# Kernel tuning notes

Hardware: AMD Instinct MI355X
Metric: run time of the kernel (lower is better)

Reference implementation:

```python
import jax, jax.numpy as jnp
import numpy as np

T = 0.07  # temperature from __init__ default


def setup_inputs() -> dict:
    key = jax.random.key(0)
    ks = jax.random.split(key, 5)
    B, D, H, E = 4096, 2048, 2048, 128
    init = lambda k, shp, fan: jax.random.normal(k, shp, dtype=jnp.float32) * (1.0 / np.sqrt(fan))
    return {
        "input1": jax.random.normal(ks[0], (B, D), dtype=jnp.float32),
        "input2": jax.random.normal(ks[1], (B, D), dtype=jnp.float32),
        "W0": init(ks[2], (D, H), D), "b0": jnp.zeros((H,), jnp.float32),
        "W1": init(ks[3], (H, H), H), "b1": jnp.zeros((H,), jnp.float32),
        "W2": init(ks[4], (H, E), H), "b2": jnp.zeros((E,), jnp.float32),
    }


def _mlp(x, W0, b0, W1, b1, W2, b2):
    # Linear -> ReLU -> Linear -> Linear (ReLU only between hidden layers)
    x = jax.nn.relu(x @ W0 + b0)
    x = x @ W1 + b1
    return x @ W2 + b2


def reference(input1, input2, W0, b0, W1, b1, W2, b2):
    B = input1.shape[0]
    e1 = _mlp(input1, W0, b0, W1, b1, W2, b2)
    e2 = _mlp(input2, W0, b0, W1, b1, W2, b2)
    feats = jnp.stack([e1, e2], axis=1)                       # [B, 2, E]
    feats = feats / jnp.linalg.norm(feats, axis=2, keepdims=True)
    # view(N,2,dim).permute(1,0,2).reshape(2N,dim): view0 rows then view1 rows
    f = jnp.concatenate([feats[:, 0], feats[:, 1]], axis=0)   # [2B, E]
    N2 = 2 * B
    sim = (f @ f.T) / T                                        # [2B, 2B]
    idx = jnp.arange(N2)
    pos = sim[idx, (idx + B) % N2]                             # partner view similarity
    # exclude self-similarity (diagonal) from the logsumexp denominator
    sim = jnp.where(jnp.eye(N2, dtype=bool), jnp.float32(-1e9), sim)
    # CE with positive at index 0 of [pos, negatives] == -pos + logsumexp(non-self)
    loss = jnp.mean(jax.nn.logsumexp(sim, axis=1) - pos)
    return loss
```

## Files before the change

kernel.cpp:

```cpp
#include <hip/hip_runtime.h>
#include <stdint.h>

typedef float f32x4 __attribute__((ext_vector_type(4)));
typedef float f32x16 __attribute__((ext_vector_type(16)));
typedef __bf16 bf16x8 __attribute__((ext_vector_type(8)));
typedef unsigned short u16;
typedef unsigned int u32;

#define INVT 14.285714285714286f

__device__ __forceinline__ u16 f2bf(float f) {
  u32 u = __float_as_uint(f);
  u32 r = (u + 0x7fffu + ((u >> 16) & 1u)) >> 16;
  return (u16)r;
}
__device__ __forceinline__ float bf2f(u16 h) { return __uint_as_float(((u32)h) << 16); }

__device__ __forceinline__ void g2l16(const void* g, void* l) {
  auto gp = reinterpret_cast<__attribute__((address_space(1))) uint32_t*>(
      reinterpret_cast<uintptr_t>(g));
  auto lp = reinterpret_cast<__attribute__((address_space(3))) uint32_t*>(
      reinterpret_cast<uintptr_t>(l));
  __builtin_amdgcn_global_load_lds(gp, lp, 16, 0, 0);
}

__global__ __launch_bounds__(256) void k_cvt2(const float* __restrict__ in1,
                                              const float* __restrict__ in2,
                                              u16* __restrict__ out) {
  int i = (blockIdx.x * 256 + threadIdx.x) * 4;
  float4 v;
  if (i < 8388608) v = *(const float4*)(in1 + i);
  else             v = *(const float4*)(in2 + (i - 8388608));
  ushort4 p;
  p.x = f2bf(v.x); p.y = f2bf(v.y); p.z = f2bf(v.z); p.w = f2bf(v.w);
  *(ushort4*)(out + i) = p;
}

__global__ __launch_bounds__(256) void k_transpose2(const float* __restrict__ w0,
                                                    u16* __restrict__ w0t,
                                                    const float* __restrict__ w1,
                                                    u16* __restrict__ w1t) {
  const float* in = blockIdx.z ? w1 : w0;
  u16* out = blockIdx.z ? w1t : w0t;
  const int R = 2048, C = 2048;
  __shared__ float t[64][65];
  const int r0 = blockIdx.y * 64, c0 = blockIdx.x * 64;
#pragma unroll
  for (int p = 0; p < 16; ++p) {
    int idx = p * 256 + threadIdx.x;
    int r = idx >> 6, c = idx & 63;
    t[r][c] = in[(size_t)(r0 + r) * C + (c0 + c)];
  }
  __syncthreads();
#pragma unroll
  for (int p = 0; p < 16; ++p) {
    int idx = p * 256 + threadIdx.x;
    int c = idx >> 6, r = idx & 63;
    out[(size_t)(c0 + c) * R + (r0 + r)] = f2bf(t[r][c]);
  }
}

__global__ __launch_bounds__(256) void k_transpose(const float* __restrict__ in,
                                                   u16* __restrict__ out, int R, int C) {
  __shared__ float t[64][65];
  const int r0 = blockIdx.y * 64, c0 = blockIdx.x * 64;
#pragma unroll
  for (int p = 0; p < 16; ++p) {
    int idx = p * 256 + threadIdx.x;
    int r = idx >> 6, c = idx & 63;
    t[r][c] = in[(size_t)(r0 + r) * C + (c0 + c)];
  }
  __syncthreads();
#pragma unroll
  for (int p = 0; p < 16; ++p) {
    int idx = p * 256 + threadIdx.x;
    int c = idx >> 6, r = idx & 63;
    out[(size_t)(c0 + c) * R + (r0 + r)] = f2bf(t[r][c]);
  }
}

__global__ __launch_bounds__(256, 2) void k_gemm(const u16* __restrict__ A, const u16* __restrict__ Bt,
                                                 const float* __restrict__ bias, u16* __restrict__ C,
                                                 int M, int N, int K, int relu) {
  __shared__ __align__(16) u16 sm[36864];
  const int tid = threadIdx.x;
  const int l = tid & 63, w = tid >> 6;
  const int wm = w >> 1, wn = w & 1;
  const int m0 = blockIdx.y * 256, n0 = blockIdx.x * 128;

  const int kb = ((l & 3) ^ ((l >> 3) & 3)) * 16;
  const char* gA = (const char*)(A + (size_t)(m0 + w * 64 + (l >> 2)) * K) + kb;
  const char* gB = (const char*)(Bt + (size_t)(n0 + w * 32 + (l >> 2)) * K) + kb;
  const size_t chRows = (size_t)16 * K * 2;

  auto issue = [&](int kcB, int stg) {
    char* base = (char*)sm + stg * 24576;
    char* dA = base + (w * 4) * 1024 + l * 16;
    char* dB = base + 16384 + (w * 2) * 1024 + l * 16;
#pragma unroll
    for (int j = 0; j < 4; ++j) g2l16(gA + j * chRows + kcB, dA + j * 1024);
#pragma unroll
    for (int j = 0; j < 2; ++j) g2l16(gB + j * chRows + kcB, dB + j * 1024);
  };

  const int lm = l & 31;
  const int c0 = l >> 5;
  const int sw = (lm >> 1) & 3;

  f32x16 acc[4][2] = {};

  auto compute = [&](int stg) {
    const u16* As = sm + stg * 12288;
    const u16* Bs = As + 8192;
#pragma unroll
    for (int t = 0; t < 2; ++t) {
      const int cc = (((t << 1) + c0) ^ sw) * 8;
      bf16x8 a4[4], b2[2];
#pragma unroll
      for (int fm = 0; fm < 4; ++fm)
        a4[fm] = *(const bf16x8*)(As + (wm * 128 + fm * 32 + lm) * 32 + cc);
#pragma unroll
      for (int fn = 0; fn < 2; ++fn)
        b2[fn] = *(const bf16x8*)(Bs + (wn * 64 + fn * 32 + lm) * 32 + cc);
#pragma unroll
      for (int fm = 0; fm < 4; ++fm)
#pragma unroll
        for (int fn = 0; fn < 2; ++fn)
          acc[fm][fn] = __builtin_amdgcn_mfma_f32_32x32x16_bf16(a4[fm], b2[fn],
                                                                acc[fm][fn], 0, 0, 0);
    }
  };

  const int NK = K >> 5;
  issue(0, 0);
  issue(64, 1);
  int st = 0;
  for (int kt = 0; kt < NK; ++kt) {
    if (kt + 1 < NK) asm volatile("s_waitcnt vmcnt(6)" ::: "memory");
    else             asm volatile("s_waitcnt vmcnt(0)" ::: "memory");
    asm volatile("s_barrier" ::: "memory");
    if (kt + 2 < NK) {
      int stp = st + 2; if (stp >= 3) stp -= 3;
      issue((kt + 2) * 64, stp);
    }
    compute(st);
    ++st; if (st == 3) st = 0;
  }

  const int colb = n0 + wn * 64 + lm;
  const int rowb = m0 + wm * 128 + 4 * c0;
#pragma unroll
  for (int fn = 0; fn < 2; ++fn) {
    const float b = bias[colb + fn * 32];
#pragma unroll
    for (int fm = 0; fm < 4; ++fm)
#pragma unroll
      for (int g = 0; g < 4; ++g)
#pragma unroll
        for (int rr = 0; rr < 4; ++rr) {
          float v = acc[fm][fn][g * 4 + rr] + b;
          if (relu) v = fmaxf(v, 0.0f);
          C[(size_t)(rowb + fm * 32 + g * 8 + rr) * N + colb + fn * 32] = f2bf(v);
        }
  }
}

__global__ __launch_bounds__(256, 2) void k_gemm_sk(const u16* __restrict__ A, const u16* __restrict__ Bt,
                                                    float* __restrict__ Ep, int K, int Ksplit) {
  __shared__ __align__(16) u16 sm[24576];
  const int tid = threadIdx.x;
  const int l = tid & 63, w = tid >> 6;
  const int wm = w >> 1, wn = w & 1;
  const int m0 = blockIdx.y * 128;
  const int split = blockIdx.x;
  const int k0s = split * Ksplit;

  const int kb = ((l & 3) ^ ((l >> 3) & 3)) * 16;
  const char* gA = (const char*)(A + (size_t)(m0 + w * 16 + (l >> 2)) * K + k0s) + kb;
  const char* gB = (const char*)(Bt + (size_t)(w * 16 + (l >> 2)) * K + k0s) + kb;
  const size_t radv = (size_t)64 * K * 2;

  auto issue = [&](int kcB, int stg) {
    char* base = (char*)sm + stg * 16384;
    char* dA = base + w * 1024 + l * 16;
    char* dB = base + 8192 + w * 1024 + l * 16;
    g2l16(gA + kcB, dA);
    g2l16(gA + radv + kcB, dA + 4096);
    g2l16(gB + kcB, dB);
    g2l16(gB + radv + kcB, dB + 4096);
  };

  const int lm = l & 31;
  const int c0 = l >> 5;
  const int sw = (lm >> 1) & 3;

  f32x16 acc[2][2] = {};

  auto compute = [&](int stg) {
    const u16* As = sm + stg * 8192;
    const u16* Bs = As + 4096;
#pragma unroll
    for (int t = 0; t < 2; ++t) {
      const int cc = (((t << 1) + c0) ^ sw) * 8;
      bf16x8 a2[2], b2[2];
#pragma unroll
      for (int fm = 0; fm < 2; ++fm) a2[fm] = *(const bf16x8*)(As + (wm * 64 + fm * 32 + lm) * 32 + cc);
#pragma unroll
      for (int fn = 0; fn < 2; ++fn) b2[fn] = *(const bf16x8*)(Bs + (wn * 64 + fn * 32 + lm) * 32 + cc);
#pragma unroll
      for (int fm = 0; fm < 2; ++fm)
#pragma unroll
        for (int fn = 0; fn < 2; ++fn)
          acc[fm][fn] = __builtin_amdgcn_mfma_f32_32x32x16_bf16(a2[fm], b2[fn],
                                                                acc[fm][fn], 0, 0, 0);
    }
  };

  const int NK = Ksplit >> 5;
  issue(0, 0);
  issue(64, 1);
  int st = 0;
  for (int kt = 0; kt < NK; ++kt) {
    if (kt + 1 < NK) asm volatile("s_waitcnt vmcnt(4)" ::: "memory");
    else             asm volatile("s_waitcnt vmcnt(0)" ::: "memory");
    asm volatile("s_barrier" ::: "memory");
    if (kt + 2 < NK) {
      int stp = st + 2; if (stp >= 3) stp -= 3;
      issue((kt + 2) * 64, stp);
    }
    compute(st);
    ++st; if (st == 3) st = 0;
  }

  const int colb = wn * 64 + lm;
  const int rowb = m0 + wm * 64 + 4 * c0;
#pragma unroll
  for (int fn = 0; fn < 2; ++fn)
#pragma unroll
    for (int fm = 0; fm < 2; ++fm)
#pragma unroll
      for (int g = 0; g < 4; ++g)
#pragma unroll
        for (int rr = 0; rr < 4; ++rr)
          Ep[((size_t)split * 8192 + rowb + fm * 32 + g * 8 + rr) * 128 + colb + fn * 32] =
              acc[fm][fn][g * 4 + rr];
}

__global__ __launch_bounds__(256) void k_norm(const float* __restrict__ Ep,
                                              const float* __restrict__ b2, u16* __restrict__ F) {
  const int l = threadIdx.x & 63, w = threadIdx.x >> 6;
  const int row = blockIdx.x * 4 + w;
  const float2* base = (const float2*)Ep + (size_t)row * 64 + l;
  float x = 0.f, y = 0.f;
#pragma unroll
  for (int s = 0; s < 4; ++s) {
    float2 t = base[(size_t)s * (8192 * 64)];
    x += t.x; y += t.y;
  }
  x += b2[l * 2]; y += b2[l * 2 + 1];
  float sq = x * x + y * y;
#pragma unroll
  for (int off = 1; off < 64; off <<= 1) sq += __shfl_xor(sq, off);
  const float inv = 1.0f / sqrtf(sq);
  F[(size_t)row * 128 + l * 2] = f2bf(x * inv);
  F[(size_t)row * 128 + l * 2 + 1] = f2bf(y * inv);
}

__global__ __launch_bounds__(256) void k_sim(const u16* __restrict__ F, float* __restrict__ Sp) {
  __shared__ __align__(16) u16 As[64 * 128];
  const int tid = threadIdx.x;
  const int l = tid & 63, w = tid >> 6;
  const int wm = w >> 1, wn = w & 1;
  const int row0 = blockIdx.y * 64;
  const int chunk = blockIdx.x;

#pragma unroll
  for (int j = 0; j < 4; ++j) {
    const int c = j * 4 + w;
    const int r = c * 4 + (l >> 4);
    const int cb = (l & 15) * 16;
    g2l16((const char*)(F + (size_t)(row0 + r) * 128) + cb, (char*)As + c * 1024 + l * 16);
  }
  asm volatile("s_waitcnt vmcnt(0)" ::: "memory");
  __syncthreads();

  bf16x8 af[2][4];
#pragma unroll
  for (int i = 0; i < 2; ++i)
#pragma unroll
    for (int s = 0; s < 4; ++s)
      af[i][s] = *(const bf16x8*)(As + (wm * 32 + i * 16 + (l & 15)) * 128 + s * 32 + (l >> 4) * 8);

  float runS[2][4] = {};
#pragma unroll 1
  for (int ct = 0; ct < 16; ++ct) {
    const int n0 = chunk * 2048 + ct * 128 + wn * 64;
    f32x4 acc[2][4] = {};
#pragma unroll
    for (int j = 0; j < 4; ++j) {
      const u16* bp = F + (size_t)(n0 + j * 16 + (l & 15)) * 128 + (l >> 4) * 8;
#pragma unroll
      for (int s = 0; s < 4; ++s) {
        bf16x8 bfr = *(const bf16x8*)(bp + s * 32);
        acc[0][j] = __builtin_amdgcn_mfma_f32_16x16x32_bf16(af[0][s], bfr, acc[0][j], 0, 0, 0);
        acc[1][j] = __builtin_amdgcn_mfma_f32_16x16x32_bf16(af[1][s], bfr, acc[1][j], 0, 0, 0);
      }
    }
#pragma unroll
    for (int i = 0; i < 2; ++i) {
      const int rb = row0 + wm * 32 + i * 16 + ((l >> 4) << 2);
#pragma unroll
      for (int r = 0; r < 4; ++r) {
        const int grow = rb + r;
        float sp = 0.f;
#pragma unroll
        for (int j = 0; j < 4; ++j) {
          const int gcol = n0 + j * 16 + (l & 15);
          float v = acc[i][j][r] * INVT;
          v = (gcol == grow) ? -1e30f : v;
          sp += __expf(v - INVT);
        }
        sp += __shfl_xor(sp, 1);
        sp += __shfl_xor(sp, 2);
        sp += __shfl_xor(sp, 4);
        sp += __shfl_xor(sp, 8);
        runS[i][r] += sp;
      }
    }
  }

  __syncthreads();
  float* red = (float*)As;
  if (wn == 0 && (l & 15) == 0) {
#pragma unroll
    for (int i = 0; i < 2; ++i)
#pragma unroll
      for (int r = 0; r < 4; ++r)
        red[wm * 32 + i * 16 + ((l >> 4) << 2) + r] = runS[i][r];
  }
  __syncthreads();
  if (wn == 1 && (l & 15) == 0) {
#pragma unroll
    for (int i = 0; i < 2; ++i)
#pragma unroll
      for (int r = 0; r < 4; ++r) {
        const int rr = wm * 32 + i * 16 + ((l >> 4) << 2) + r;
        Sp[(size_t)chunk * 8192 + row0 + rr] = red[rr] + runS[i][r];
      }
  }
}

__global__ __launch_bounds__(256) void k_combine(const float* __restrict__ Sp,
                                                 const u16* __restrict__ F,
                                                 float* __restrict__ out) {
  const int r = blockIdx.x * 256 + threadIdx.x;
  float S = Sp[r] + Sp[8192 + r] + Sp[2 * 8192 + r] + Sp[3 * 8192 + r];
  const float lse = INVT + logf(S);
  const int par = (r + 4096) & 8191;
  const u16* a = F + (size_t)r * 128;
  const u16* b = F + (size_t)par * 128;
  float dot = 0.f;
#pragma unroll 8
  for (int k = 0; k < 128; ++k) dot = fmaf(bf2f(a[k]), bf2f(b[k]), dot);
  float contrib = lse - dot * INVT;
#pragma unroll
  for (int off = 1; off < 64; off <<= 1) contrib += __shfl_xor(contrib, off);
  if ((threadIdx.x & 63) == 0) atomicAdd(out, contrib * (1.0f / 8192.0f));
}

extern "C" void kernel_launch(void* const* d_in, const int* in_sizes, int n_in,
                              void* d_out, int out_size, void* d_ws, size_t ws_size,
                              hipStream_t stream) {
  const float* input1 = (const float*)d_in[0];
  const float* input2 = (const float*)d_in[1];
  const float* W0 = (const float*)d_in[2];
  const float* b0 = (const float*)d_in[3];
  const float* W1 = (const float*)d_in[4];
  const float* b1 = (const float*)d_in[5];
  const float* W2 = (const float*)d_in[6];
  const float* b2 = (const float*)d_in[7];
  float* out = (float*)d_out;
  char* ws = (char*)d_ws;

  u16* Xb = (u16*)(ws + 0);
  u16* H1 = (u16*)(ws + 33554432);
  u16* W0T = (u16*)(ws + 67108864);
  u16* W1T = (u16*)(ws + 75497472);
  float* Ep = (float*)(ws + 67108864);
  u16* W2T = (u16*)(ws + 83886080);
  u16* Ff = (u16*)(ws + 84410368);
  float* Sp = (float*)(ws + 86507520);
  u16* H2 = Xb;

  hipMemsetAsync(d_out, 0, sizeof(float), stream);
  k_cvt2<<<16384, 256, 0, stream>>>(input1, input2, Xb);
  k_transpose2<<<dim3(32, 32, 2), 256, 0, stream>>>(W0, W0T, W1, W1T);
  k_transpose<<<dim3(2, 32), 256, 0, stream>>>(W2, W2T, 2048, 128);
  k_gemm<<<dim3(16, 32), 256, 0, stream>>>(Xb, W0T, b0, H1, 8192, 2048, 2048, 1);
  k_gemm<<<dim3(16, 32), 256, 0, stream>>>(H1, W1T, b1, H2, 8192, 2048, 2048, 0);
  k_gemm_sk<<<dim3(4, 64), 256, 0, stream>>>(H2, W2T, Ep, 2048, 512);
  k_norm<<<2048, 256, 0, stream>>>(Ep, b2, Ff);
  k_sim<<<dim3(4, 128), 256, 0, stream>>>(Ff, Sp);
  k_combine<<<32, 256, 0, stream>>>(Sp, Ff, out);
}
```

Baseline: 374.6 us.

## Restructure similarity kernel with 128x128 tiles, LDS double-buffering and 32x32 MFMA

Rewrites the similarity/logsumexp kernel so each block computes a 128-row tile against 1024 columns. The column tiles are double-buffered in swizzled LDS through async global-to-LDS loads, where before B fragments were read straight from global memory. It switches to 32x32x16 MFMA, folds the scale into exp2 with a single fma, and only checks for the diagonal on tiles that can contain it. It also defers the cross-lane reduction to the end and doubles the column split to 8 partial sums, moving the partial buffer into the workspace slot freed by W2T. The cost is more LDS (64KB) and more registers, limited by a launch bound of two blocks per CU.

```diff
diff --git a/kernel.cpp b/kernel.cpp
--- a/kernel.cpp
+++ b/kernel.cpp
@@ -8,6 +8,7 @@
 typedef unsigned int u32;
 
 #define INVT 14.285714285714286f
+#define L2E  1.4426950408889634f
 
 __device__ __forceinline__ u16 f2bf(float f) {
   u32 u = __float_as_uint(f);
@@ -266,86 +267,127 @@
   F[(size_t)row * 128 + l * 2 + 1] = f2bf(y * inv);
 }
 
-__global__ __launch_bounds__(256) void k_sim(const u16* __restrict__ F, float* __restrict__ Sp) {
-  __shared__ __align__(16) u16 As[64 * 128];
+__global__ __launch_bounds__(256, 2) void k_sim(const u16* __restrict__ F, float* __restrict__ Sp) {
+  __shared__ __align__(16) u16 sm[32768];
   const int tid = threadIdx.x;
   const int l = tid & 63, w = tid >> 6;
   const int wm = w >> 1, wn = w & 1;
-  const int row0 = blockIdx.y * 64;
-  const int chunk = blockIdx.x;
-
-#pragma unroll
-  for (int j = 0; j < 4; ++j) {
-    const int c = j * 4 + w;
-    const int r = c * 4 + (l >> 4);
-    const int cb = (l & 15) * 16;
-    g2l16((const char*)(F + (size_t)(row0 + r) * 128) + cb, (char*)As + c * 1024 + l * 16);
-  }
+  const int lm = l & 31, c0 = l >> 5;
+  const int r0 = blockIdx.y * 128;
+  const int cb0 = blockIdx.x * 1024;
+
+  u16* B0 = sm;
+  u16* AB1 = sm + 16384;
+
+  const int srow0 = tid >> 4;
+  const int schunk = tid & 15;
+  auto stage = [&](const u16* src, u16* dst) {
+#pragma unroll
+    for (int j = 0; j < 8; ++j) {
+      const int row = j * 16 + srow0;
+      const int lc = schunk ^ (row & 7);
+      g2l16((const char*)(src + (size_t)row * 128) + lc * 16,
+            (char*)dst + j * 4096 + tid * 16);
+    }
+  };
+
+  stage(F + (size_t)r0 * 128, AB1);
   asm volatile("s_waitcnt vmcnt(0)" ::: "memory");
   __syncthreads();
 
-  bf16x8 af[2][4];
-#pragma unroll
-  for (int i = 0; i < 2; ++i)
-#pragma unroll
-    for (int s = 0; s < 4; ++s)
-      af[i][s] = *(const bf16x8*)(As + (wm * 32 + i * 16 + (l & 15)) * 128 + s * 32 + (l >> 4) * 8);
-
-  float runS[2][4] = {};
+  bf16x8 a[2][8];
+#pragma unroll
+  for (int fm = 0; fm < 2; ++fm) {
+    const int ra = wm * 64 + fm * 32 + lm;
+#pragma unroll
+    for (int kf = 0; kf < 8; ++kf)
+      a[fm][kf] = *(const bf16x8*)(AB1 + ra * 128 + (((kf << 1) + c0) ^ (ra & 7)) * 8);
+  }
+  asm volatile("s_waitcnt lgkmcnt(0)" ::: "memory");
+
+  stage(F + (size_t)cb0 * 128, B0);
+
+  const float S2 = INVT * L2E;
+  const int rB = wn * 64 + lm;
+  f32x16 runS[2] = {};
+
 #pragma unroll 1
-  for (int ct = 0; ct < 16; ++ct) {
-    const int n0 = chunk * 2048 + ct * 128 + wn * 64;
-    f32x4 acc[2][4] = {};
-#pragma unroll
-    for (int j = 0; j < 4; ++j) {
-      const u16* bp = F + (size_t)(n0 + j * 16 + (l & 15)) * 128 + (l >> 4) * 8;
-#pragma unroll
-      for (int s = 0; s < 4; ++s) {
-        bf16x8 bfr = *(const bf16x8*)(bp + s * 32);
-        acc[0][j] = __builtin_amdgcn_mfma_f32_16x16x32_bf16(af[0][s], bfr, acc[0][j], 0, 0, 0);
-        acc[1][j] = __builtin_amdgcn_mfma_f32_16x16x32_bf16(af[1][s], bfr, acc[1][j], 0, 0, 0);
-      }
-    }
-#pragma unroll
-    for (int i = 0; i < 2; ++i) {
-      const int rb = row0 + wm * 32 + i * 16 + ((l >> 4) << 2);
-#pragma unroll
-      for (int r = 0; r < 4; ++r) {
-        const int grow = rb + r;
-        float sp = 0.f;
-#pragma unroll
-        for (int j = 0; j < 4; ++j) {
-          const int gcol = n0 + j * 16 + (l & 15);
-          float v = acc[i][j][r] * INVT;
-          v = (gcol == grow) ? -1e30f : v;
-          sp += __expf(v - INVT);
+  for (int p = 0; p < 8; ++p) {
+    asm volatile("s_waitcnt vmcnt(0)" ::: "memory");
+    asm volatile("s_barrier" ::: "memory");
+    if (p < 7) stage(F + (size_t)(cb0 + (p + 1) * 128) * 128, (p & 1) ? B0 : AB1);
+    const u16* Bs = (p & 1) ? AB1 : B0;
+
+    f32x16 acc[2][2] = {};
+#pragma unroll
+    for (int kf = 0; kf < 8; ++kf) {
+      const int kc = (kf << 1) + c0;
+      bf16x8 b0v = *(const bf16x8*)(Bs + rB * 128 + (kc ^ (rB & 7)) * 8);
+      bf16x8 b1v = *(const bf16x8*)(Bs + (rB + 32) * 128 + (kc ^ ((rB + 32) & 7)) * 8);
+      acc[0][0] = __builtin_amdgcn_mfma_f32_32x32x16_bf16(a[0][kf], b0v, acc[0][0], 0, 0, 0);
+      acc[0][1] = __builtin_amdgcn_mfma_f32_32x32x16_bf16(a[0][kf], b1v, acc[0][1], 0, 0, 0);
+      acc[1][0] = __builtin_amdgcn_mfma_f32_32x32x16_bf16(a[1][kf], b0v, acc[1][0], 0, 0, 0);
+      acc[1][1] = __builtin_amdgcn_mfma_f32_32x32x16_bf16(a[1][kf], b1v, acc[1][1], 0, 0, 0);
+    }
+
+    const int cp = cb0 + p * 128;
+    if (cp == r0) {
+#pragma unroll
+      for (int fm = 0; fm < 2; ++fm)
+#pragma unroll
+        for (int fn = 0; fn < 2; ++fn) {
+          const int rcol = wn * 64 + fn * 32 + lm;
+#pragma unroll
+          for (int r = 0; r < 16; ++r) {
+            const int rrow = wm * 64 + fm * 32 + (r & 3) + 8 * (r >> 2) + 4 * c0;
+            float e = exp2f(fmaf(acc[fm][fn][r], S2, -S2));
+            if (rrow == rcol) e = 0.f;
+            runS[fm][r] += e;
+          }
         }
-        sp += __shfl_xor(sp, 1);
-        sp += __shfl_xor(sp, 2);
-        sp += __shfl_xor(sp, 4);
-        sp += __shfl_xor(sp, 8);
-        runS[i][r] += sp;
-      }
-    }
-  }
+    } else {
+#pragma unroll
+      for (int fm = 0; fm < 2; ++fm)
+#pragma unroll
+        for (int fn = 0; fn < 2; ++fn)
+#pragma unroll
+          for (int r = 0; r < 16; ++r)
+            runS[fm][r] += exp2f(fmaf(acc[fm][fn][r], S2, -S2));
+    }
+  }
+
+#pragma unroll
+  for (int fm = 0; fm < 2; ++fm)
+#pragma unroll
+    for (int r = 0; r < 16; ++r) {
+      float s = runS[fm][r];
+      s += __shfl_xor(s, 1);
+      s += __shfl_xor(s, 2);
+      s += __shfl_xor(s, 4);
+      s += __shfl_xor(s, 8);
+      s += __shfl_xor(s, 16);
+      runS[fm][r] = s;
+    }
 
   __syncthreads();
-  float* red = (float*)As;
-  if (wn == 0 && (l & 15) == 0) {
-#pragma unroll
-    for (int i = 0; i < 2; ++i)
-#pragma unroll
-      for (int r = 0; r < 4; ++r)
-        red[wm * 32 + i * 16 + ((l >> 4) << 2) + r] = runS[i][r];
+  float* red = (float*)sm;
+  if (wn == 0) {
+    if (lm == 0) {
+#pragma unroll
+      for (int fm = 0; fm < 2; ++fm)
+#pragma unroll
+        for (int r = 0; r < 16; ++r)
+          red[wm * 64 + fm * 32 + (r & 3) + 8 * (r >> 2) + 4 * c0] = runS[fm][r];
+    }
   }
   __syncthreads();
-  if (wn == 1 && (l & 15) == 0) {
-#pragma unroll
-    for (int i = 0; i < 2; ++i)
-#pragma unroll
-      for (int r = 0; r < 4; ++r) {
-        const int rr = wm * 32 + i * 16 + ((l >> 4) << 2) + r;
-        Sp[(size_t)chunk * 8192 + row0 + rr] = red[rr] + runS[i][r];
+  if (wn == 1 && lm == 0) {
+#pragma unroll
+    for (int fm = 0; fm < 2; ++fm)
+#pragma unroll
+      for (int r = 0; r < 16; ++r) {
+        const int rr = wm * 64 + fm * 32 + (r & 3) + 8 * (r >> 2) + 4 * c0;
+        Sp[(size_t)blockIdx.x * 8192 + r0 + rr] = red[rr] + runS[fm][r];
       }
   }
 }
@@ -354,7 +396,9 @@
                                                  const u16* __restrict__ F,
                                                  float* __restrict__ out) {
   const int r = blockIdx.x * 256 + threadIdx.x;
-  float S = Sp[r] + Sp[8192 + r] + Sp[2 * 8192 + r] + Sp[3 * 8192 + r];
+  float S = 0.f;
+#pragma unroll
+  for (int c = 0; c < 8; ++c) S += Sp[c * 8192 + r];
   const float lse = INVT + logf(S);
   const int par = (r + 4096) & 8191;
   const u16* a = F + (size_t)r * 128;
@@ -388,8 +432,8 @@
   u16* W1T = (u16*)(ws + 75497472);
   float* Ep = (float*)(ws + 67108864);
   u16* W2T = (u16*)(ws + 83886080);
+  float* Sp = (float*)(ws + 83886080);
   u16* Ff = (u16*)(ws + 84410368);
-  float* Sp = (float*)(ws + 86507520);
   u16* H2 = Xb;
 
   hipMemsetAsync(d_out, 0, sizeof(float), stream);
@@ -400,6 +444,6 @@
   k_gemm<<<dim3(16, 32), 256, 0, stream>>>(H1, W1T, b1, H2, 8192, 2048, 2048, 0);
   k_gemm_sk<<<dim3(4, 64), 256, 0, stream>>>(H2, W2T, Ep, 2048, 512);
   k_norm<<<2048, 256, 0, stream>>>(Ep, b2, Ff);
-  k_sim<<<dim3(4, 128), 256, 0, stream>>>(Ff, Sp);
+  k_sim<<<dim3(8, 64), 256, 0, stream>>>(Ff, Sp);
   k_combine<<<32, 256, 0, stream>>>(Sp, Ff, out);
 }
```

New measurement: 346.6 us. 7.5% less time.
